# Kernel optimization log

Measured on AMD Instinct MI355X. Metric: run time of the kernel, lower is better.

Reference implementation:

```python
import jax, jax.numpy as jnp
import numpy as np

B, T, F, H, C = 256, 14, 1024, 1024, 2513


def lstm_step(Wih, Whh, bih, bhh, x, h, c):
    # PyTorch LSTM cell: gate order i, f, g, o
    g = x @ Wih.T + bih + h @ Whh.T + bhh
    i, f, gg, o = jnp.split(g, 4, axis=-1)
    i = jax.nn.sigmoid(i)
    f = jax.nn.sigmoid(f)
    gg = jnp.tanh(gg)
    o = jax.nn.sigmoid(o)
    c = f * c + i * gg
    h = o * jnp.tanh(c)
    return h, c


def setup_inputs() -> dict:
    key = jax.random.key(0)
    ks = jax.random.split(key, 11)
    s = 1.0 / np.sqrt(H)
    u = lambda k, shape: jax.random.uniform(k, shape, jnp.float32, -s, s)
    return {
        "inputs": jax.random.normal(ks[0], (B, T, F), jnp.float32),
        "roll_Wih": u(ks[1], (4 * H, F)),
        "roll_Whh": u(ks[2], (4 * H, H)),
        "roll_bih": u(ks[3], (4 * H,)),
        "roll_bhh": u(ks[4], (4 * H,)),
        "unroll_Wih": u(ks[5], (4 * H, F)),
        "unroll_Whh": u(ks[6], (4 * H, H)),
        "unroll_bih": u(ks[7], (4 * H,)),
        "unroll_bhh": u(ks[8], (4 * H,)),
        "cls_W": u(ks[9], (C, H)),
        "cls_b": u(ks[10], (C,)),
    }


def reference(inputs, roll_Wih, roll_Whh, roll_bih, roll_bhh,
              unroll_Wih, unroll_Whh, unroll_bih, unroll_bhh, cls_W, cls_b):
    x_t = jnp.transpose(inputs, (1, 0, 2))  # [T, B, F]

    # Rolling LSTM: scan over time, keep hidden/cell at every step
    h0 = jnp.zeros((B, H), inputs.dtype)
    c0 = jnp.zeros((B, H), inputs.dtype)

    def roll(carry, xt):
        h, c = carry
        h, c = lstm_step(roll_Wih, roll_Whh, roll_bih, roll_bhh, xt, h, c)
        return (h, c), (h, c)

    _, (hs, cs) = jax.lax.scan(roll, (h0, c0), x_t)  # each [T, B, H]

    # Unrolling LSTM: for each t, feed inputs[t] repeated (T - t + 1) times,
    # starting from (hs[t], cs[t]). Vectorized over t: run T+1 steps for all
    # branches with constant per-branch input x_t[t], then pick step (T - t).
    def unroll(carry, _):
        h, c = carry  # [T, B, H]
        h, c = lstm_step(unroll_Wih, unroll_Whh, unroll_bih, unroll_bhh, x_t, h, c)
        return (h, c), h

    _, h_all = jax.lax.scan(unroll, (hs, cs), None, length=T + 1)  # [T+1, T, B, H]
    t_idx = jnp.arange(T)
    h_n = h_all[T - t_idx, t_idx]  # [T, B, H], last output of each branch

    x = jnp.transpose(h_n, (1, 0, 2))  # [B, T, H]
    y = x @ cls_W.T + cls_b  # [B, T, C]
    return y
```

## Files before the change

kernel.cpp:

```cpp
#include <hip/hip_runtime.h>

#define DEVFN __device__ __forceinline__

typedef __bf16 bf16x8 __attribute__((ext_vector_type(8)));
typedef float floatx4 __attribute__((ext_vector_type(4)));
typedef unsigned short us4 __attribute__((ext_vector_type(4)));


DEVFN unsigned short f2bf(float x) {
    union { float f; unsigned u; } v; v.f = x;
    v.u += 0x7FFFu + ((v.u >> 16) & 1u);
    return (unsigned short)(v.u >> 16);
}

DEVFN float bf2f(unsigned short s) {
    union { unsigned u; float f; } v; v.u = ((unsigned)s) << 16; return v.f;
}

DEVFN float sigm(float x) { return 1.f / (1.f + __expf(-x)); }
DEVFN float tanh_fast(float x) { float t = __expf(2.f * x); return 1.f - 2.f / (t + 1.f); }

DEVFN void gload_lds16(const unsigned short* g, unsigned short* l) {
    __builtin_amdgcn_global_load_lds(
        (__attribute__((address_space(1))) unsigned int*)g,
        (__attribute__((address_space(3))) unsigned int*)l, 16, 0, 0);
}

#define CFENCE asm volatile("" ::: "memory")


__global__ __launch_bounds__(256) void transpose_bt(const float* __restrict__ in,
                                                    unsigned short* __restrict__ out) {
    int idx = blockIdx.x * 256 + threadIdx.x;
    int k4 = (idx & 255) << 2;
    int row = idx >> 8;
    int t = row >> 8, b = row & 255;
    float4 v = *(const float4*)(in + (size_t)(b * 14 + t) * 1024 + k4);
    us4 o = {f2bf(v.x), f2bf(v.y), f2bf(v.z), f2bf(v.w)};
    *(us4*)(out + (size_t)row * 1024 + k4) = o;
}

__global__ __launch_bounds__(256) void conv_w4(const float* __restrict__ s0, const float* __restrict__ s1,
                                               const float* __restrict__ s2, const float* __restrict__ s3,
                                               unsigned short* __restrict__ d0, unsigned short* __restrict__ d1,
                                               unsigned short* __restrict__ d2, unsigned short* __restrict__ d3) {
    int t = blockIdx.x * 256 + threadIdx.x;
    int which = t >> 20;
    int off = (t & 1048575) << 2;
    const float* s = (which == 0) ? s0 : (which == 1) ? s1 : (which == 2) ? s2 : s3;
    unsigned short* d = (which == 0) ? d0 : (which == 1) ? d1 : (which == 2) ? d2 : d3;
    float4 v = *(const float4*)(s + off);
    us4 o = {f2bf(v.x), f2bf(v.y), f2bf(v.z), f2bf(v.w)};
    *(us4*)(d + off) = o;
}

__global__ __launch_bounds__(256) void conv_cls(const float* __restrict__ in,
                                                unsigned short* __restrict__ out) {
    int t = blockIdx.x * 256 + threadIdx.x;
    int off = t << 2;
    us4 o = {0, 0, 0, 0};
    if (off < 2573312) {
        float4 v = *(const float4*)(in + off);
        o = (us4){f2bf(v.x), f2bf(v.y), f2bf(v.z), f2bf(v.w)};
    }
    *(us4*)(out + off) = o;
}

__global__ __launch_bounds__(256) void bias_interleave(const float* __restrict__ a,
                                                       const float* __restrict__ b,
                                                       float* __restrict__ o4, int n) {
    int i = blockIdx.x * 256 + threadIdx.x;
    if (i < n) {
        int g = i >> 10, h = i & 1023;
        o4[h * 4 + g] = a[i] + b[i];
    }
}

template <int MODE>
__global__ __launch_bounds__(512, 2)
void lstm_mega(const unsigned short* __restrict__ A1,
               const unsigned short* __restrict__ W1,
               const unsigned short* __restrict__ W2,
               const unsigned short* __restrict__ pre4b,
               const float* __restrict__ bias4a,
               const float* __restrict__ bias4b,
               const float* __restrict__ c_in,
               float* __restrict__ c_out,
               unsigned short* __restrict__ h_out,
               unsigned short* __restrict__ h_alt, int retire_t,
               unsigned short* __restrict__ g1,
               unsigned short* __restrict__ g2,
               const float* __restrict__ clsb,
               float* __restrict__ outp) {
    __shared__ __align__(16) unsigned short lds[2][32768];

    const int tid = threadIdx.x;
    const int b = blockIdx.x;
    int bx, by;
    if (MODE == 2) {
        bx = b % 10; by = b / 10;
    } else if (MODE == 4) {
        int sel = (b >> 3) & 3;
        bx = ((sel & 1) << 4) + ((b & 7) << 1) + (sel >> 1);
        by = b >> 5;
    } else {
        bx = ((b & 7) << 1) + ((b >> 3) & 1);
        by = b >> 4;
    }
    const int m0 = by * 256;
    const int n0h = (MODE == 4) ? (bx & 15) * 64 : bx * 64;
    const int n0c = bx * 256;
    const int lane = tid & 63;
    const int wv = tid >> 6;
    const int wm = wv >> 2, wn = wv & 3;
    const int r16 = lane & 15;
    const int kg = lane >> 4;

    const unsigned short* Ws = (MODE == 4 && (bx >> 4)) ? W2 : W1;

    auto st = [&](int t, int s) {
        if (t >= 16) return;
        const int ko = t * 64;
        if (s < 4) {
            int rb = s * 64 + (tid >> 3);
            int kq = tid & 7;
            int kqg = kq ^ (rb & 7);
            int wr;
            if (MODE == 2) wr = n0c + rb;
            else wr = ((rb >> 4) & 3) * 1024 + n0h + ((rb >> 6) << 4) + (rb & 15);
            gload_lds16(Ws + (size_t)wr * 1024 + ko + kqg * 8,
                        &lds[t & 1][16384 + s * 4096 + tid * 8]);
        } else {
            int q = s - 4;
            int lr = tid >> 3;
            int rlog = ((lr >> 5) << 7) + q * 32 + (lr & 31);
            int kq = tid & 7;
            int kqg = kq ^ (lr & 7);
            gload_lds16(A1 + (size_t)(m0 + rlog) * 1024 + ko + kqg * 8,
                        &lds[t & 1][q * 4096 + tid * 8]);
        }
    };

    floatx4 acc[8][4];
#pragma unroll
    for (int i = 0; i < 8; ++i)
#pragma unroll
        for (int j = 0; j < 4; ++j) acc[i][j] = {0.f, 0.f, 0.f, 0.f};

#pragma unroll
    for (int s = 0; s < 8; ++s) st(0, s);
#pragma unroll
    for (int s = 0; s < 6; ++s) st(1, s);
    asm volatile("s_waitcnt vmcnt(6)" ::: "memory");
    __builtin_amdgcn_s_barrier();
    CFENCE;

    for (int v = 0; v < 8; ++v) {
        const int te = 2 * v;
        bf16x8 bfr[4][2];
#pragma unroll
        for (int p = 0; p < 8; ++p) {
            const int q = p & 3;
            const int buf = p >> 2;
            if (p == 0) {
                asm volatile("s_waitcnt vmcnt(6)" ::: "memory");
            } else if (p == 4) {
                if (v == 7) asm volatile("s_waitcnt vmcnt(0)" ::: "memory");
                else        asm volatile("s_waitcnt vmcnt(6)" ::: "memory");
            }
            if (q == 0) {
#pragma unroll
                for (int j = 0; j < 4; ++j)
#pragma unroll
                    for (int kk = 0; kk < 2; ++kk) {
                        int rb = wn * 64 + j * 16 + r16;
                        bfr[j][kk] = *(const bf16x8*)&lds[buf][16384 + rb * 64 +
                                         (((kk << 2) + kg) ^ (rb & 7)) * 8];
                    }
            }
            bf16x8 a[2][2];
#pragma unroll
            for (int i = 0; i < 2; ++i)
#pragma unroll
                for (int kk = 0; kk < 2; ++kk) {
                    int ra = q * 64 + wm * 32 + i * 16 + r16;
                    a[i][kk] = *(const bf16x8*)&lds[buf][ra * 64 +
                                   (((kk << 2) + kg) ^ (ra & 7)) * 8];
                }
            {
                int tt = (p == 0) ? te + 1 : (p <= 4 ? te + 2 : te + 3);
                int s0 = (p == 0 || p == 4) ? 6 : ((p == 1 || p == 5) ? 0 :
                         ((p == 2 || p == 6) ? 2 : 4));
                st(tt, s0);
                st(tt, s0 + 1);
            }
            __builtin_amdgcn_s_barrier();
            CFENCE;
            __builtin_amdgcn_s_setprio(1);
#pragma unroll
            for (int i = 0; i < 2; ++i)
#pragma unroll
                for (int j = 0; j < 4; ++j)
#pragma unroll
                    for (int kk = 0; kk < 2; ++kk)
                        acc[q * 2 + i][j] = __builtin_amdgcn_mfma_f32_16x16x32_bf16(
                            a[i][kk], bfr[j][kk], acc[q * 2 + i][j], 0, 0, 0);
            __builtin_amdgcn_s_setprio(0);
            __builtin_amdgcn_s_barrier();
            CFENCE;
        }
    }

    if (MODE == 2) {
#pragma unroll
        for (int i = 0; i < 8; ++i)
#pragma unroll
            for (int j = 0; j < 4; ++j)
#pragma unroll
                for (int rg = 0; rg < 4; ++rg) {
                    int m = m0 + wm * 128 + i * 16 + kg * 4 + rg;
                    int gn = n0c + wn * 64 + j * 16 + r16;
                    if (gn < 2513) {
                        int bb = m & 255, tt = m >> 8;
                        __builtin_nontemporal_store(acc[i][j][rg] + clsb[gn],
                                                    outp + (size_t)(bb * 14 + tt) * 2513 + gn);
                    }
                }
        return;
    }

    const int h = n0h + wn * 16 + r16;

    if (MODE == 4) {
        const int half = bx >> 4;
        unsigned short* gsel = half ? g2 : g1;
        const float* bsel = half ? bias4b : bias4a;
        const bool cell0 = (half == 1) && (by == 0);
        float4 bv = *(const float4*)(bsel + (size_t)h * 4);
#pragma unroll
        for (int i = 0; i < 8; ++i)
#pragma unroll
            for (int rg = 0; rg < 4; ++rg) {
                int m = m0 + wm * 128 + i * 16 + kg * 4 + rg;
                size_t mh = (size_t)m * 1024 + h;
                float gi_ = acc[i][0][rg] + bv.x;
                float gf_ = acc[i][1][rg] + bv.y;
                float gg_ = acc[i][2][rg] + bv.z;
                float go_ = acc[i][3][rg] + bv.w;
                if (cell0) {
                    float iv = sigm(gi_), ov = sigm(go_);
                    float gv = tanh_fast(gg_);
                    float cn = iv * gv;
                    float hn = ov * tanh_fast(cn);
                    c_out[mh] = cn;
                    h_out[mh] = f2bf(hn);
                } else {
                    us4 o = {f2bf(gi_), f2bf(gf_), f2bf(gg_), f2bf(go_)};
                    *(us4*)(gsel + mh * 4) = o;
                }
            }
        return;
    }

    unsigned short* hw = (by == retire_t) ? h_alt : h_out;
#pragma unroll
    for (int i = 0; i < 8; ++i)
#pragma unroll
        for (int rg = 0; rg < 4; ++rg) {
            int m = m0 + wm * 128 + i * 16 + kg * 4 + rg;
            size_t mh = (size_t)m * 1024 + h;
            us4 pv = *(const us4*)(pre4b + mh * 4);
            float gi_ = acc[i][0][rg] + bf2f(pv.x);
            float gf_ = acc[i][1][rg] + bf2f(pv.y);
            float gg_ = acc[i][2][rg] + bf2f(pv.z);
            float go_ = acc[i][3][rg] + bf2f(pv.w);
            float co = c_in[mh];
            float iv = sigm(gi_), fv = sigm(gf_);
            float gv = tanh_fast(gg_), ov = sigm(go_);
            float cn = fv * co + iv * gv;
            float hn = ov * tanh_fast(cn);
            c_out[mh] = cn;
            hw[mh] = f2bf(hn);
        }
}

template <int MODE, int NH>
__global__ __launch_bounds__(256, 2)
void lstm_big(const unsigned short* __restrict__ A1,
              const unsigned short* __restrict__ W1,
              const unsigned short* __restrict__ pre4b,
              const float* __restrict__ c_in,
              float* __restrict__ c_out,
              unsigned short* __restrict__ h_out,
              unsigned short* __restrict__ h_alt, int retire_t, int gx) {
    constexpr int BROWS = 4 * NH;
    constexpr int FN = BROWS / 32;
    constexpr int BISS = BROWS / 64;
    constexpr int LOADS = 2 + BISS;
    constexpr int ASH = 4096;
    constexpr int BSH = BROWS * 32;
    constexpr int HH = NH / 32;

    __shared__ __align__(16) unsigned short lds[3][ASH + BSH];

    const int tid = threadIdx.x;
    const int b = blockIdx.x;
    const int bx = ((b & 7) << 2) + ((b >> 3) & 3);
    const int by = b >> 5;
    const int m0 = by * 128;
    const int n0h = bx * NH;
    const int lane = tid & 63;
    const int wv = tid >> 6;
    const int wm = wv >> 1, wn = wv & 1;
    const int r16 = lane & 15;
    const int kg = lane >> 4;
    (void)gx;

    auto stage = [&](int u, int buf) {
        const int ko = u * 32;
#pragma unroll
        for (int is = 0; is < 2; ++is) {
            int c = is * 256 + tid;
            int row = c >> 2, kq = c & 3;
            int kqg = kq ^ ((row >> 1) & 3);
            gload_lds16(A1 + (size_t)(m0 + row) * 1024 + ko + kqg * 8, &lds[buf][c * 8]);
        }
#pragma unroll
        for (int is = 0; is < BISS; ++is) {
            int c = is * 256 + tid;
            int row = c >> 2, kq = c & 3;
            int kqg = kq ^ ((row >> 1) & 3);
            int wr = ((row >> 4) & 3) * 1024 + n0h + ((row >> 6) << 4) + (row & 15);
            gload_lds16(W1 + (size_t)wr * 1024 + ko + kqg * 8, &lds[buf][ASH + c * 8]);
        }
    };

    floatx4 acc[4][FN];
#pragma unroll
    for (int i = 0; i < 4; ++i)
#pragma unroll
        for (int j = 0; j < FN; ++j) acc[i][j] = {0.f, 0.f, 0.f, 0.f};

    stage(0, 0);
    stage(1, 1);
    stage(2, 2);
    asm volatile("s_waitcnt vmcnt(%0)" :: "n"(2 * LOADS) : "memory");
    __builtin_amdgcn_s_barrier();
    CFENCE;

    int cur = 0;
    for (int u = 0; u < 32; ++u) {
        bf16x8 a[4], bfr[FN];
#pragma unroll
        for (int i = 0; i < 4; ++i) {
            int row = wm * 64 + i * 16 + r16;
            a[i] = *(const bf16x8*)&lds[cur][row * 32 + (kg ^ ((row >> 1) & 3)) * 8];
        }
#pragma unroll
        for (int j = 0; j < FN; ++j) {
            int row = wn * (BROWS / 2) + j * 16 + r16;
            bfr[j] = *(const bf16x8*)&lds[cur][ASH + row * 32 + (kg ^ ((row >> 1) & 3)) * 8];
        }
        __builtin_amdgcn_s_setprio(1);
#pragma unroll
        for (int i = 0; i < 4; ++i)
#pragma unroll
            for (int j = 0; j < FN; ++j)
                acc[i][j] = __builtin_amdgcn_mfma_f32_16x16x32_bf16(a[i], bfr[j], acc[i][j], 0, 0, 0);
        __builtin_amdgcn_s_setprio(0);

        if (u < 31) {
            __builtin_amdgcn_s_barrier();
            if (u < 29) {
                stage(u + 3, cur);
                asm volatile("s_waitcnt vmcnt(%0)" :: "n"(2 * LOADS) : "memory");
            } else if (u == 29) {
                asm volatile("s_waitcnt vmcnt(%0)" :: "n"(LOADS) : "memory");
            } else {
                asm volatile("s_waitcnt vmcnt(0)" ::: "memory");
            }
            __builtin_amdgcn_s_barrier();
            CFENCE;
        }
        cur = (cur == 2) ? 0 : cur + 1;
    }

    unsigned short* hw = ((m0 >> 8) == retire_t) ? h_alt : h_out;
#pragma unroll
    for (int hh = 0; hh < HH; ++hh) {
        const int h = n0h + wn * (NH / 2) + hh * 16 + r16;
#pragma unroll
        for (int i = 0; i < 4; ++i)
#pragma unroll
            for (int rg = 0; rg < 4; ++rg) {
                int m = m0 + wm * 64 + i * 16 + kg * 4 + rg;
                size_t mh = (size_t)m * 1024 + h;
                us4 pv = *(const us4*)(pre4b + mh * 4);
                float gi_ = acc[i][hh * 4 + 0][rg] + bf2f(pv.x);
                float gf_ = acc[i][hh * 4 + 1][rg] + bf2f(pv.y);
                float gg_ = acc[i][hh * 4 + 2][rg] + bf2f(pv.z);
                float go_ = acc[i][hh * 4 + 3][rg] + bf2f(pv.w);
                float co = c_in[mh];
                float iv = sigm(gi_), fv = sigm(gf_);
                float gv = tanh_fast(gg_), ov = sigm(go_);
                float cn = fv * co + iv * gv;
                float hn = ov * tanh_fast(cn);
                c_out[mh] = cn;
                hw[mh] = f2bf(hn);
            }
    }
}

__global__ __launch_bounds__(256)
void lstm_small(const unsigned short* __restrict__ A1, const unsigned short* __restrict__ W1,
                const unsigned short* __restrict__ pre4b,
                const float* __restrict__ c_in,
                float* __restrict__ c_out,
                unsigned short* __restrict__ h_out,
                unsigned short* __restrict__ h_alt, int retire_t) {
    constexpr int ATILE = 32 * 64;
    constexpr int LOADS = 5;

    __shared__ __align__(16) unsigned short lds[4][ATILE + 8192];

    const int tid = threadIdx.x;
    const int b = blockIdx.x;
    const int bx = ((b & 7) << 2) + ((b >> 3) & 3);
    const int by = b >> 5;
    const int m0 = by * 32;
    const int n0 = bx * 32;
    const int lane = tid & 63;
    const int wv = tid >> 6;
    const int wm = wv >> 1, wn = wv & 1;
    const int r16 = lane & 15;
    const int kg = lane >> 4;

    auto stage = [&](int kt, int buf) {
        const int ko = kt * 64;
        {
            int c = tid;
            int row = c >> 3, kq = c & 7, kqg = kq ^ (row & 7);
            gload_lds16(A1 + (size_t)(m0 + row) * 1024 + ko + kqg * 8, &lds[buf][c * 8]);
        }
#pragma unroll
        for (int is = 0; is < 4; ++is) {
            int c = is * 256 + tid;
            int row = c >> 3, kq = c & 7, kqg = kq ^ (row & 7);
            int wr = ((row >> 4) & 3) * 1024 + n0 + ((row >> 6) << 4) + (row & 15);
            gload_lds16(W1 + (size_t)wr * 1024 + ko + kqg * 8, &lds[buf][ATILE + c * 8]);
        }
    };

    floatx4 acc[4];
#pragma unroll
    for (int j = 0; j < 4; ++j) acc[j] = {0.f, 0.f, 0.f, 0.f};

    stage(0, 0);
    stage(1, 1);
    stage(2, 2);
    asm volatile("s_waitcnt vmcnt(%0)" :: "n"(2 * LOADS) : "memory");
    __builtin_amdgcn_s_barrier();
    CFENCE;

#pragma unroll 4
    for (int u = 0; u < 16; ++u) {
        const int cur = u & 3;
#pragma unroll
        for (int kk = 0; kk < 2; ++kk) {
            bf16x8 a, bfr[4];
            const int kqg = kk * 4 + kg;
            {
                int row = wm * 16 + r16;
                a = *(const bf16x8*)&lds[cur][row * 64 + (kqg ^ (row & 7)) * 8];
            }
#pragma unroll
            for (int j = 0; j < 4; ++j) {
                int row = wn * 64 + j * 16 + r16;
                bfr[j] = *(const bf16x8*)&lds[cur][ATILE + row * 64 + (kqg ^ (row & 7)) * 8];
            }
#pragma unroll
            for (int j = 0; j < 4; ++j)
                acc[j] = __builtin_amdgcn_mfma_f32_16x16x32_bf16(a, bfr[j], acc[j], 0, 0, 0);
        }
        if (u < 15) {
            __builtin_amdgcn_s_barrier();
            if (u < 13) {
                stage(u + 3, (u + 3) & 3);
                asm volatile("s_waitcnt vmcnt(%0)" :: "n"(2 * LOADS) : "memory");
            } else if (u == 13) {
                asm volatile("s_waitcnt vmcnt(%0)" :: "n"(LOADS) : "memory");
            } else {
                asm volatile("s_waitcnt vmcnt(0)" ::: "memory");
            }
            __builtin_amdgcn_s_barrier();
            CFENCE;
        }
    }

    const int h = n0 + wn * 16 + r16;
    unsigned short* hw = ((m0 >> 8) == retire_t) ? h_alt : h_out;

#pragma unroll
    for (int rg = 0; rg < 4; ++rg) {
        int m = m0 + wm * 16 + kg * 4 + rg;
        size_t mh = (size_t)m * 1024 + h;
        us4 pv = *(const us4*)(pre4b + mh * 4);
        float gi_ = acc[0][rg] + bf2f(pv.x);
        float gf_ = acc[1][rg] + bf2f(pv.y);
        float gg_ = acc[2][rg] + bf2f(pv.z);
        float go_ = acc[3][rg] + bf2f(pv.w);
        float co = c_in[mh];
        float iv = sigm(gi_), fv = sigm(gf_);
        float gv = tanh_fast(gg_), ov = sigm(go_);
        float cn = fv * co + iv * gv;
        float hn = ov * tanh_fast(cn);
        c_out[mh] = cn;
        hw[mh] = f2bf(hn);
    }
}


extern "C" void kernel_launch(void* const* d_in, const int* in_sizes, int n_in,
                              void* d_out, int out_size, void* d_ws, size_t ws_size,
                              hipStream_t stream) {
    (void)in_sizes; (void)n_in; (void)out_size; (void)ws_size;
    const float* inputs   = (const float*)d_in[0];
    const float* roll_Wih = (const float*)d_in[1];
    const float* roll_Whh = (const float*)d_in[2];
    const float* roll_bih = (const float*)d_in[3];
    const float* roll_bhh = (const float*)d_in[4];
    const float* un_Wih   = (const float*)d_in[5];
    const float* un_Whh   = (const float*)d_in[6];
    const float* un_bih   = (const float*)d_in[7];
    const float* un_bhh   = (const float*)d_in[8];
    const float* cls_Wf   = (const float*)d_in[9];
    const float* cls_b    = (const float*)d_in[10];
    float* out = (float*)d_out;

    char* ws = (char*)d_ws;
    size_t off = 0;
    auto alloc = [&](size_t bytes) -> char* {
        char* p = ws + off;
        off += (bytes + 255) & ~(size_t)255;
        return p;
    };
    unsigned short* xt   = (unsigned short*)alloc(3584ull * 1024 * 2);
    unsigned short* rWih = (unsigned short*)alloc(4096ull * 1024 * 2);
    unsigned short* rWhh = (unsigned short*)alloc(4096ull * 1024 * 2);
    unsigned short* uWih = (unsigned short*)alloc(4096ull * 1024 * 2);
    unsigned short* uWhh = (unsigned short*)alloc(4096ull * 1024 * 2);
    unsigned short* cWp  = (unsigned short*)alloc(2560ull * 1024 * 2);
    float* rbias4 = (float*)alloc(1024 * 4 * 4);
    float* ubias4 = (float*)alloc(1024 * 4 * 4);
    unsigned short* XpreB  = (unsigned short*)alloc(3584ull * 4096 * 2);
    unsigned short* XrollB = (unsigned short*)alloc(3584ull * 4096 * 2);
    float* uc     = (float*)alloc(3584ull * 1024 * 4);
    unsigned short* hb0    = (unsigned short*)alloc(3584ull * 1024 * 2);
    unsigned short* hb1    = (unsigned short*)alloc(3584ull * 1024 * 2);
    unsigned short* hfinal = (unsigned short*)alloc(3584ull * 1024 * 2);

    const size_t SF = 256 * 1024;

    transpose_bt<<<3584, 256, 0, stream>>>(inputs, xt);
    conv_w4<<<16384, 256, 0, stream>>>(roll_Wih, roll_Whh, un_Wih, un_Whh,
                                       rWih, rWhh, uWih, uWhh);
    conv_cls<<<2560, 256, 0, stream>>>(cls_Wf, cWp);
    bias_interleave<<<16, 256, 0, stream>>>(roll_bih, roll_bhh, rbias4, 4096);
    bias_interleave<<<16, 256, 0, stream>>>(un_bih, un_bhh, ubias4, 4096);

    lstm_mega<4><<<448, 512, 0, stream>>>(
        xt, uWih, rWih, nullptr, ubias4, rbias4,
        nullptr, uc, hb0, nullptr, -1, XpreB, XrollB, nullptr, nullptr);

    for (int t = 1; t < 14; ++t) {
        lstm_small<<<256, 256, 0, stream>>>(
            hb0 + (size_t)(t - 1) * SF, rWhh,
            XrollB + (size_t)t * SF * 4,
            uc + (size_t)(t - 1) * SF, uc + (size_t)t * SF,
            hb0 + (size_t)t * SF, nullptr, -1);
    }

    for (int s = 0; s <= 14; ++s) {
        int nb = (15 - s < 14) ? (15 - s) : 14;
        int M = nb * 256;
        const unsigned short* hsrc = (s & 1) ? hb1 : hb0;
        unsigned short* hdst = (s & 1) ? hb0 : hb1;
        int rt = (s >= 1) ? (14 - s) : -1;
        if (M >= 2304) {
            lstm_mega<1><<<nb * 16, 512, 0, stream>>>(
                hsrc, uWhh, nullptr, XpreB, nullptr, nullptr,
                uc, uc, hdst, hfinal, rt, nullptr, nullptr, nullptr, nullptr);
        } else if (M >= 1024) {
            lstm_big<1, 32><<<M / 4, 256, 0, stream>>>(
                hsrc, uWhh, XpreB, uc, uc, hdst, hfinal, rt, 32);
        } else {
            lstm_small<<<M, 256, 0, stream>>>(
                hsrc, uWhh, XpreB, uc, uc, hdst, hfinal, rt);
        }
    }

    lstm_mega<2><<<140, 512, 0, stream>>>(
        hfinal, cWp, nullptr, nullptr, nullptr, nullptr,
        nullptr, nullptr, nullptr, nullptr, -1, nullptr, nullptr, cls_b, out);
}
```

Measured before the change: 684.6 us.

## Fuse rolling and unrolling LSTM steps into wavefront superstep launches

Replaces the serial rolling-LSTM loop (13 small launches) followed by 15 unrolling launches with 15 combined superstep launches. Each superstep runs rolling step u alongside every unrolling branch that is already ready, so branch t starts as soon as hs[t] exists. Branch step 0 reads h and c straight from the rolling buffers, and the final step skips the cell-state write. This cuts the launch count and overlaps the two recurrences. In exchange, every step now uses the 256x256-tile kernel, so early supersteps with few blocks leave most CUs idle, and the rolling path loses the wide-grid small kernel.

```diff
diff --git a/kernel.cpp b/kernel.cpp
--- a/kernel.cpp
+++ b/kernel.cpp
@@ -81,13 +81,10 @@
 void lstm_mega(const unsigned short* __restrict__ A1,
                const unsigned short* __restrict__ W1,
                const unsigned short* __restrict__ W2,
-               const unsigned short* __restrict__ pre4b,
                const float* __restrict__ bias4a,
                const float* __restrict__ bias4b,
-               const float* __restrict__ c_in,
                float* __restrict__ c_out,
                unsigned short* __restrict__ h_out,
-               unsigned short* __restrict__ h_alt, int retire_t,
                unsigned short* __restrict__ g1,
                unsigned short* __restrict__ g2,
                const float* __restrict__ clsb,
@@ -99,16 +96,13 @@
     int bx, by;
     if (MODE == 2) {
         bx = b % 10; by = b / 10;
-    } else if (MODE == 4) {
+    } else {
         int sel = (b >> 3) & 3;
         bx = ((sel & 1) << 4) + ((b & 7) << 1) + (sel >> 1);
         by = b >> 5;
-    } else {
-        bx = ((b & 7) << 1) + ((b >> 3) & 1);
-        by = b >> 4;
     }
     const int m0 = by * 256;
-    const int n0h = (MODE == 4) ? (bx & 15) * 64 : bx * 64;
+    const int n0h = (MODE == 4) ? (bx & 15) * 64 : 0;
     const int n0c = bx * 256;
     const int lane = tid & 63;
     const int wv = tid >> 6;
@@ -230,293 +224,200 @@
     }
 
     const int h = n0h + wn * 16 + r16;
-
-    if (MODE == 4) {
-        const int half = bx >> 4;
-        unsigned short* gsel = half ? g2 : g1;
-        const float* bsel = half ? bias4b : bias4a;
-        const bool cell0 = (half == 1) && (by == 0);
-        float4 bv = *(const float4*)(bsel + (size_t)h * 4);
-#pragma unroll
-        for (int i = 0; i < 8; ++i)
-#pragma unroll
-            for (int rg = 0; rg < 4; ++rg) {
-                int m = m0 + wm * 128 + i * 16 + kg * 4 + rg;
-                size_t mh = (size_t)m * 1024 + h;
-                float gi_ = acc[i][0][rg] + bv.x;
-                float gf_ = acc[i][1][rg] + bv.y;
-                float gg_ = acc[i][2][rg] + bv.z;
-                float go_ = acc[i][3][rg] + bv.w;
-                if (cell0) {
-                    float iv = sigm(gi_), ov = sigm(go_);
-                    float gv = tanh_fast(gg_);
-                    float cn = iv * gv;
-                    float hn = ov * tanh_fast(cn);
-                    c_out[mh] = cn;
-                    h_out[mh] = f2bf(hn);
-                } else {
-                    us4 o = {f2bf(gi_), f2bf(gf_), f2bf(gg_), f2bf(go_)};
-                    *(us4*)(gsel + mh * 4) = o;
-                }
-            }
-        return;
-    }
-
-    unsigned short* hw = (by == retire_t) ? h_alt : h_out;
+    const int half = bx >> 4;
+    unsigned short* gsel = half ? g2 : g1;
+    const float* bsel = half ? bias4b : bias4a;
+    const bool cell0 = (half == 1) && (by == 0);
+    float4 bv = *(const float4*)(bsel + (size_t)h * 4);
 #pragma unroll
     for (int i = 0; i < 8; ++i)
 #pragma unroll
         for (int rg = 0; rg < 4; ++rg) {
             int m = m0 + wm * 128 + i * 16 + kg * 4 + rg;
             size_t mh = (size_t)m * 1024 + h;
-            us4 pv = *(const us4*)(pre4b + mh * 4);
+            float gi_ = acc[i][0][rg] + bv.x;
+            float gf_ = acc[i][1][rg] + bv.y;
+            float gg_ = acc[i][2][rg] + bv.z;
+            float go_ = acc[i][3][rg] + bv.w;
+            if (cell0) {
+                float iv = sigm(gi_), ov = sigm(go_);
+                float gv = tanh_fast(gg_);
+                float cn = iv * gv;
+                float hn = ov * tanh_fast(cn);
+                c_out[mh] = cn;
+                h_out[mh] = f2bf(hn);
+            } else {
+                us4 o = {f2bf(gi_), f2bf(gf_), f2bf(gg_), f2bf(go_)};
+                *(us4*)(gsel + mh * 4) = o;
+            }
+        }
+}
+
+__global__ __launch_bounds__(512, 2)
+void superstep(unsigned short* __restrict__ hroll,
+               const unsigned short* __restrict__ hsrc,
+               unsigned short* __restrict__ hdst,
+               unsigned short* __restrict__ hfinal,
+               float* __restrict__ croll,
+               float* __restrict__ cunr,
+               const unsigned short* __restrict__ XpreB,
+               const unsigned short* __restrict__ XrollB,
+               const unsigned short* __restrict__ uWhh,
+               const unsigned short* __restrict__ rWhh,
+               int u, int nbU) {
+    __shared__ __align__(16) unsigned short lds[2][32768];
+
+    const size_t SF = 256 * 1024;
+    const int tid = threadIdx.x;
+    const int id = blockIdx.x;
+    const bool isRoll = (id >= nbU * 16);
+    const int rid = isRoll ? id - nbU * 16 : id;
+    const int bx = ((rid & 7) << 1) + ((rid >> 3) & 1);
+    const int t = isRoll ? u : (rid >> 4);
+    const int s = u - 1 - t;
+
+    const unsigned short* A1;
+    const unsigned short* Ws;
+    const unsigned short* pre;
+    const float* cin;
+    float* cout;
+    unsigned short* hout;
+    bool skipC = false;
+    if (isRoll) {
+        A1 = hroll + (size_t)(u - 1) * SF;
+        Ws = rWhh;
+        pre = XrollB + (size_t)u * SF * 4;
+        cin = croll + (size_t)(u - 1) * SF;
+        cout = croll + (size_t)u * SF;
+        hout = hroll + (size_t)u * SF;
+    } else {
+        A1 = (s == 0 ? hroll : hsrc) + (size_t)t * SF;
+        Ws = uWhh;
+        pre = XpreB + (size_t)t * SF * 4;
+        cin = (s == 0 ? croll : cunr) + (size_t)t * SF;
+        cout = cunr + (size_t)t * SF;
+        hout = (u == 15 ? hfinal : hdst) + (size_t)t * SF;
+        skipC = (u == 15);
+    }
+
+    const int n0h = bx * 64;
+    const int lane = tid & 63;
+    const int wv = tid >> 6;
+    const int wm = wv >> 2, wn = wv & 3;
+    const int r16 = lane & 15;
+    const int kg = lane >> 4;
+
+    auto st = [&](int tt, int ss) {
+        if (tt >= 16) return;
+        const int ko = tt * 64;
+        if (ss < 4) {
+            int rb = ss * 64 + (tid >> 3);
+            int kq = tid & 7;
+            int kqg = kq ^ (rb & 7);
+            int wr = ((rb >> 4) & 3) * 1024 + n0h + ((rb >> 6) << 4) + (rb & 15);
+            gload_lds16(Ws + (size_t)wr * 1024 + ko + kqg * 8,
+                        &lds[tt & 1][16384 + ss * 4096 + tid * 8]);
+        } else {
+            int q = ss - 4;
+            int lr = tid >> 3;
+            int rlog = ((lr >> 5) << 7) + q * 32 + (lr & 31);
+            int kq = tid & 7;
+            int kqg = kq ^ (lr & 7);
+            gload_lds16(A1 + (size_t)rlog * 1024 + ko + kqg * 8,
+                        &lds[tt & 1][q * 4096 + tid * 8]);
+        }
+    };
+
+    floatx4 acc[8][4];
+#pragma unroll
+    for (int i = 0; i < 8; ++i)
+#pragma unroll
+        for (int j = 0; j < 4; ++j) acc[i][j] = {0.f, 0.f, 0.f, 0.f};
+
+#pragma unroll
+    for (int ss = 0; ss < 8; ++ss) st(0, ss);
+#pragma unroll
+    for (int ss = 0; ss < 6; ++ss) st(1, ss);
+    asm volatile("s_waitcnt vmcnt(6)" ::: "memory");
+    __builtin_amdgcn_s_barrier();
+    CFENCE;
+
+    for (int v = 0; v < 8; ++v) {
+        const int te = 2 * v;
+        bf16x8 bfr[4][2];
+#pragma unroll
+        for (int p = 0; p < 8; ++p) {
+            const int q = p & 3;
+            const int buf = p >> 2;
+            if (p == 0) {
+                asm volatile("s_waitcnt vmcnt(6)" ::: "memory");
+            } else if (p == 4) {
+                if (v == 7) asm volatile("s_waitcnt vmcnt(0)" ::: "memory");
+                else        asm volatile("s_waitcnt vmcnt(6)" ::: "memory");
+            }
+            if (q == 0) {
+#pragma unroll
+                for (int j = 0; j < 4; ++j)
+#pragma unroll
+                    for (int kk = 0; kk < 2; ++kk) {
+                        int rb = wn * 64 + j * 16 + r16;
+                        bfr[j][kk] = *(const bf16x8*)&lds[buf][16384 + rb * 64 +
+                                         (((kk << 2) + kg) ^ (rb & 7)) * 8];
+                    }
+            }
+            bf16x8 a[2][2];
+#pragma unroll
+            for (int i = 0; i < 2; ++i)
+#pragma unroll
+                for (int kk = 0; kk < 2; ++kk) {
+                    int ra = q * 64 + wm * 32 + i * 16 + r16;
+                    a[i][kk] = *(const bf16x8*)&lds[buf][ra * 64 +
+                                   (((kk << 2) + kg) ^ (ra & 7)) * 8];
+                }
+            {
+                int tt = (p == 0) ? te + 1 : (p <= 4 ? te + 2 : te + 3);
+                int s0 = (p == 0 || p == 4) ? 6 : ((p == 1 || p == 5) ? 0 :
+                         ((p == 2 || p == 6) ? 2 : 4));
+                st(tt, s0);
+                st(tt, s0 + 1);
+            }
+            __builtin_amdgcn_s_barrier();
+            CFENCE;
+            __builtin_amdgcn_s_setprio(1);
+#pragma unroll
+            for (int i = 0; i < 2; ++i)
+#pragma unroll
+                for (int j = 0; j < 4; ++j)
+#pragma unroll
+                    for (int kk = 0; kk < 2; ++kk)
+                        acc[q * 2 + i][j] = __builtin_amdgcn_mfma_f32_16x16x32_bf16(
+                            a[i][kk], bfr[j][kk], acc[q * 2 + i][j], 0, 0, 0);
+            __builtin_amdgcn_s_setprio(0);
+            __builtin_amdgcn_s_barrier();
+            CFENCE;
+        }
+    }
+
+    const int h = n0h + wn * 16 + r16;
+#pragma unroll
+    for (int i = 0; i < 8; ++i)
+#pragma unroll
+        for (int rg = 0; rg < 4; ++rg) {
+            int m = wm * 128 + i * 16 + kg * 4 + rg;
+            size_t mh = (size_t)m * 1024 + h;
+            us4 pv = *(const us4*)(pre + mh * 4);
             float gi_ = acc[i][0][rg] + bf2f(pv.x);
             float gf_ = acc[i][1][rg] + bf2f(pv.y);
             float gg_ = acc[i][2][rg] + bf2f(pv.z);
             float go_ = acc[i][3][rg] + bf2f(pv.w);
-            float co = c_in[mh];
+            float co = cin[mh];
             float iv = sigm(gi_), fv = sigm(gf_);
             float gv = tanh_fast(gg_), ov = sigm(go_);
             float cn = fv * co + iv * gv;
             float hn = ov * tanh_fast(cn);
-            c_out[mh] = cn;
-            hw[mh] = f2bf(hn);
-        }
-}
-
-template <int MODE, int NH>
-__global__ __launch_bounds__(256, 2)
-void lstm_big(const unsigned short* __restrict__ A1,
-              const unsigned short* __restrict__ W1,
-              const unsigned short* __restrict__ pre4b,
-              const float* __restrict__ c_in,
-              float* __restrict__ c_out,
-              unsigned short* __restrict__ h_out,
-              unsigned short* __restrict__ h_alt, int retire_t, int gx) {
-    constexpr int BROWS = 4 * NH;
-    constexpr int FN = BROWS / 32;
-    constexpr int BISS = BROWS / 64;
-    constexpr int LOADS = 2 + BISS;
-    constexpr int ASH = 4096;
-    constexpr int BSH = BROWS * 32;
-    constexpr int HH = NH / 32;
-
-    __shared__ __align__(16) unsigned short lds[3][ASH + BSH];
-
-    const int tid = threadIdx.x;
-    const int b = blockIdx.x;
-    const int bx = ((b & 7) << 2) + ((b >> 3) & 3);
-    const int by = b >> 5;
-    const int m0 = by * 128;
-    const int n0h = bx * NH;
-    const int lane = tid & 63;
-    const int wv = tid >> 6;
-    const int wm = wv >> 1, wn = wv & 1;
-    const int r16 = lane & 15;
-    const int kg = lane >> 4;
-    (void)gx;
-
-    auto stage = [&](int u, int buf) {
-        const int ko = u * 32;
-#pragma unroll
-        for (int is = 0; is < 2; ++is) {
-            int c = is * 256 + tid;
-            int row = c >> 2, kq = c & 3;
-            int kqg = kq ^ ((row >> 1) & 3);
-            gload_lds16(A1 + (size_t)(m0 + row) * 1024 + ko + kqg * 8, &lds[buf][c * 8]);
-        }
-#pragma unroll
-        for (int is = 0; is < BISS; ++is) {
-            int c = is * 256 + tid;
-            int row = c >> 2, kq = c & 3;
-            int kqg = kq ^ ((row >> 1) & 3);
-            int wr = ((row >> 4) & 3) * 1024 + n0h + ((row >> 6) << 4) + (row & 15);
-            gload_lds16(W1 + (size_t)wr * 1024 + ko + kqg * 8, &lds[buf][ASH + c * 8]);
-        }
-    };
-
-    floatx4 acc[4][FN];
-#pragma unroll
-    for (int i = 0; i < 4; ++i)
-#pragma unroll
-        for (int j = 0; j < FN; ++j) acc[i][j] = {0.f, 0.f, 0.f, 0.f};
-
-    stage(0, 0);
-    stage(1, 1);
-    stage(2, 2);
-    asm volatile("s_waitcnt vmcnt(%0)" :: "n"(2 * LOADS) : "memory");
-    __builtin_amdgcn_s_barrier();
-    CFENCE;
-
-    int cur = 0;
-    for (int u = 0; u < 32; ++u) {
-        bf16x8 a[4], bfr[FN];
-#pragma unroll
-        for (int i = 0; i < 4; ++i) {
-            int row = wm * 64 + i * 16 + r16;
-            a[i] = *(const bf16x8*)&lds[cur][row * 32 + (kg ^ ((row >> 1) & 3)) * 8];
-        }
-#pragma unroll
-        for (int j = 0; j < FN; ++j) {
-            int row = wn * (BROWS / 2) + j * 16 + r16;
-            bfr[j] = *(const bf16x8*)&lds[cur][ASH + row * 32 + (kg ^ ((row >> 1) & 3)) * 8];
-        }
-        __builtin_amdgcn_s_setprio(1);
-#pragma unroll
-        for (int i = 0; i < 4; ++i)
-#pragma unroll
-            for (int j = 0; j < FN; ++j)
-                acc[i][j] = __builtin_amdgcn_mfma_f32_16x16x32_bf16(a[i], bfr[j], acc[i][j], 0, 0, 0);
-        __builtin_amdgcn_s_setprio(0);
-
-        if (u < 31) {
-            __builtin_amdgcn_s_barrier();
-            if (u < 29) {
-                stage(u + 3, cur);
-                asm volatile("s_waitcnt vmcnt(%0)" :: "n"(2 * LOADS) : "memory");
-            } else if (u == 29) {
-                asm volatile("s_waitcnt vmcnt(%0)" :: "n"(LOADS) : "memory");
-            } else {
-                asm volatile("s_waitcnt vmcnt(0)" ::: "memory");
-            }
-            __builtin_amdgcn_s_barrier();
-            CFENCE;
-        }
-        cur = (cur == 2) ? 0 : cur + 1;
-    }
-
-    unsigned short* hw = ((m0 >> 8) == retire_t) ? h_alt : h_out;
-#pragma unroll
-    for (int hh = 0; hh < HH; ++hh) {
-        const int h = n0h + wn * (NH / 2) + hh * 16 + r16;
-#pragma unroll
-        for (int i = 0; i < 4; ++i)
-#pragma unroll
-            for (int rg = 0; rg < 4; ++rg) {
-                int m = m0 + wm * 64 + i * 16 + kg * 4 + rg;
-                size_t mh = (size_t)m * 1024 + h;
-                us4 pv = *(const us4*)(pre4b + mh * 4);
-                float gi_ = acc[i][hh * 4 + 0][rg] + bf2f(pv.x);
-                float gf_ = acc[i][hh * 4 + 1][rg] + bf2f(pv.y);
-                float gg_ = acc[i][hh * 4 + 2][rg] + bf2f(pv.z);
-                float go_ = acc[i][hh * 4 + 3][rg] + bf2f(pv.w);
-                float co = c_in[mh];
-                float iv = sigm(gi_), fv = sigm(gf_);
-                float gv = tanh_fast(gg_), ov = sigm(go_);
-                float cn = fv * co + iv * gv;
-                float hn = ov * tanh_fast(cn);
-                c_out[mh] = cn;
-                hw[mh] = f2bf(hn);
-            }
-    }
-}
-
-__global__ __launch_bounds__(256)
-void lstm_small(const unsigned short* __restrict__ A1, const unsigned short* __restrict__ W1,
-                const unsigned short* __restrict__ pre4b,
-                const float* __restrict__ c_in,
-                float* __restrict__ c_out,
-                unsigned short* __restrict__ h_out,
-                unsigned short* __restrict__ h_alt, int retire_t) {
-    constexpr int ATILE = 32 * 64;
-    constexpr int LOADS = 5;
-
-    __shared__ __align__(16) unsigned short lds[4][ATILE + 8192];
-
-    const int tid = threadIdx.x;
-    const int b = blockIdx.x;
-    const int bx = ((b & 7) << 2) + ((b >> 3) & 3);
-    const int by = b >> 5;
-    const int m0 = by * 32;
-    const int n0 = bx * 32;
-    const int lane = tid & 63;
-    const int wv = tid >> 6;
-    const int wm = wv >> 1, wn = wv & 1;
-    const int r16 = lane & 15;
-    const int kg = lane >> 4;
-
-    auto stage = [&](int kt, int buf) {
-        const int ko = kt * 64;
-        {
-            int c = tid;
-            int row = c >> 3, kq = c & 7, kqg = kq ^ (row & 7);
-            gload_lds16(A1 + (size_t)(m0 + row) * 1024 + ko + kqg * 8, &lds[buf][c * 8]);
-        }
-#pragma unroll
-        for (int is = 0; is < 4; ++is) {
-            int c = is * 256 + tid;
-            int row = c >> 3, kq = c & 7, kqg = kq ^ (row & 7);
-            int wr = ((row >> 4) & 3) * 1024 + n0 + ((row >> 6) << 4) + (row & 15);
-            gload_lds16(W1 + (size_t)wr * 1024 + ko + kqg * 8, &lds[buf][ATILE + c * 8]);
-        }
-    };
-
-    floatx4 acc[4];
-#pragma unroll
-    for (int j = 0; j < 4; ++j) acc[j] = {0.f, 0.f, 0.f, 0.f};
-
-    stage(0, 0);
-    stage(1, 1);
-    stage(2, 2);
-    asm volatile("s_waitcnt vmcnt(%0)" :: "n"(2 * LOADS) : "memory");
-    __builtin_amdgcn_s_barrier();
-    CFENCE;
-
-#pragma unroll 4
-    for (int u = 0; u < 16; ++u) {
-        const int cur = u & 3;
-#pragma unroll
-        for (int kk = 0; kk < 2; ++kk) {
-            bf16x8 a, bfr[4];
-            const int kqg = kk * 4 + kg;
-            {
-                int row = wm * 16 + r16;
-                a = *(const bf16x8*)&lds[cur][row * 64 + (kqg ^ (row & 7)) * 8];
-            }
-#pragma unroll
-            for (int j = 0; j < 4; ++j) {
-                int row = wn * 64 + j * 16 + r16;
-                bfr[j] = *(const bf16x8*)&lds[cur][ATILE + row * 64 + (kqg ^ (row & 7)) * 8];
-            }
-#pragma unroll
-            for (int j = 0; j < 4; ++j)
-                acc[j] = __builtin_amdgcn_mfma_f32_16x16x32_bf16(a, bfr[j], acc[j], 0, 0, 0);
-        }
-        if (u < 15) {
-            __builtin_amdgcn_s_barrier();
-            if (u < 13) {
-                stage(u + 3, (u + 3) & 3);
-                asm volatile("s_waitcnt vmcnt(%0)" :: "n"(2 * LOADS) : "memory");
-            } else if (u == 13) {
-                asm volatile("s_waitcnt vmcnt(%0)" :: "n"(LOADS) : "memory");
-            } else {
-                asm volatile("s_waitcnt vmcnt(0)" ::: "memory");
-            }
-            __builtin_amdgcn_s_barrier();
-            CFENCE;
-        }
-    }
-
-    const int h = n0 + wn * 16 + r16;
-    unsigned short* hw = ((m0 >> 8) == retire_t) ? h_alt : h_out;
-
-#pragma unroll
-    for (int rg = 0; rg < 4; ++rg) {
-        int m = m0 + wm * 16 + kg * 4 + rg;
-        size_t mh = (size_t)m * 1024 + h;
-        us4 pv = *(const us4*)(pre4b + mh * 4);
-        float gi_ = acc[0][rg] + bf2f(pv.x);
-        float gf_ = acc[1][rg] + bf2f(pv.y);
-        float gg_ = acc[2][rg] + bf2f(pv.z);
-        float go_ = acc[3][rg] + bf2f(pv.w);
-        float co = c_in[mh];
-        float iv = sigm(gi_), fv = sigm(gf_);
-        float gv = tanh_fast(gg_), ov = sigm(go_);
-        float cn = fv * co + iv * gv;
-        float hn = ov * tanh_fast(cn);
-        c_out[mh] = cn;
-        hw[mh] = f2bf(hn);
-    }
+            if (!skipC) cout[mh] = cn;
+            hout[mh] = f2bf(hn);
+        }
 }
 
 
@@ -554,12 +455,12 @@
     float* ubias4 = (float*)alloc(1024 * 4 * 4);
     unsigned short* XpreB  = (unsigned short*)alloc(3584ull * 4096 * 2);
     unsigned short* XrollB = (unsigned short*)alloc(3584ull * 4096 * 2);
-    float* uc     = (float*)alloc(3584ull * 1024 * 4);
-    unsigned short* hb0    = (unsigned short*)alloc(3584ull * 1024 * 2);
-    unsigned short* hb1    = (unsigned short*)alloc(3584ull * 1024 * 2);
+    float* croll = (float*)alloc(3584ull * 1024 * 4);
+    float* cunr  = (float*)alloc(3584ull * 1024 * 4);
+    unsigned short* hroll  = (unsigned short*)alloc(3584ull * 1024 * 2);
+    unsigned short* hp0    = (unsigned short*)alloc(3584ull * 1024 * 2);
+    unsigned short* hp1    = (unsigned short*)alloc(3584ull * 1024 * 2);
     unsigned short* hfinal = (unsigned short*)alloc(3584ull * 1024 * 2);
-
-    const size_t SF = 256 * 1024;
 
     transpose_bt<<<3584, 256, 0, stream>>>(inputs, xt);
     conv_w4<<<16384, 256, 0, stream>>>(roll_Wih, roll_Whh, un_Wih, un_Whh,
@@ -569,37 +470,20 @@
     bias_interleave<<<16, 256, 0, stream>>>(un_bih, un_bhh, ubias4, 4096);
 
     lstm_mega<4><<<448, 512, 0, stream>>>(
-        xt, uWih, rWih, nullptr, ubias4, rbias4,
-        nullptr, uc, hb0, nullptr, -1, XpreB, XrollB, nullptr, nullptr);
-
-    for (int t = 1; t < 14; ++t) {
-        lstm_small<<<256, 256, 0, stream>>>(
-            hb0 + (size_t)(t - 1) * SF, rWhh,
-            XrollB + (size_t)t * SF * 4,
-            uc + (size_t)(t - 1) * SF, uc + (size_t)t * SF,
-            hb0 + (size_t)t * SF, nullptr, -1);
-    }
-
-    for (int s = 0; s <= 14; ++s) {
-        int nb = (15 - s < 14) ? (15 - s) : 14;
-        int M = nb * 256;
-        const unsigned short* hsrc = (s & 1) ? hb1 : hb0;
-        unsigned short* hdst = (s & 1) ? hb0 : hb1;
-        int rt = (s >= 1) ? (14 - s) : -1;
-        if (M >= 2304) {
-            lstm_mega<1><<<nb * 16, 512, 0, stream>>>(
-                hsrc, uWhh, nullptr, XpreB, nullptr, nullptr,
-                uc, uc, hdst, hfinal, rt, nullptr, nullptr, nullptr, nullptr);
-        } else if (M >= 1024) {
-            lstm_big<1, 32><<<M / 4, 256, 0, stream>>>(
-                hsrc, uWhh, XpreB, uc, uc, hdst, hfinal, rt, 32);
-        } else {
-            lstm_small<<<M, 256, 0, stream>>>(
-                hsrc, uWhh, XpreB, uc, uc, hdst, hfinal, rt);
-        }
+        xt, uWih, rWih, ubias4, rbias4,
+        croll, hroll, XpreB, XrollB, nullptr, nullptr);
+
+    for (int u = 1; u <= 15; ++u) {
+        int nbU = (u < 14) ? u : 14;
+        int grid = nbU * 16 + ((u <= 13) ? 16 : 0);
+        const unsigned short* hsrc = (u & 1) ? hp1 : hp0;
+        unsigned short* hdst       = (u & 1) ? hp0 : hp1;
+        superstep<<<grid, 512, 0, stream>>>(
+            hroll, hsrc, hdst, hfinal, croll, cunr,
+            XpreB, XrollB, uWhh, rWhh, u, nbU);
     }
 
     lstm_mega<2><<<140, 512, 0, stream>>>(
-        hfinal, cWp, nullptr, nullptr, nullptr, nullptr,
-        nullptr, nullptr, nullptr, nullptr, -1, nullptr, nullptr, cls_b, out);
-}
+        hfinal, cWp, nullptr, nullptr, nullptr,
+        nullptr, nullptr, nullptr, nullptr, cls_b, out);
+}
```

Result: slower. 721.7 us (+5.4%).
